# Kernel optimization log

Hardware: AMD Instinct MI355X
Metric: run time of the kernel (lower is better)

## Reference

```python
import jax, jax.numpy as jnp
import numpy as np

B, L = 8, 128
STATE_DIM, ACT_DIM = 6, 3
E = 256
D_MODEL = 256
N_LAYER = 4
D_INNER = 512   # expand=2
D_STATE = 16
DT_RANK = 16    # ceil(d_model/16)
D_CONV = 4
MAX_EP_LEN = 300
EPS = 1e-5


def rmsnorm(x, w):
    return x * jax.lax.rsqrt(jnp.mean(x * x, axis=-1, keepdims=True) + EPS) * w


def mamba_mixer(x, in_W, conv_w, conv_b, xproj_W, dt_W, dt_b, A_log, Dp, out_W):
    # x: (B, Lp, D_MODEL)
    bsz, Lp, _ = x.shape
    di = conv_w.shape[0]
    n = A_log.shape[-1]
    rk = dt_W.shape[0]
    xz = x @ in_W                              # (B, Lp, 2*di)
    xc, z = jnp.split(xz, 2, axis=-1)
    # depthwise causal conv1d, kernel D_CONV
    xc_t = xc.transpose(0, 2, 1)               # (B, di, Lp)
    xc_t = jax.lax.conv_general_dilated(
        xc_t, conv_w[:, None, :], (1,), [(D_CONV - 1, 0)],
        feature_group_count=di,
        dimension_numbers=('NCH', 'OIH', 'NCH')) + conv_b[None, :, None]
    xc = jax.nn.silu(xc_t.transpose(0, 2, 1))  # (B, Lp, di)
    proj = xc @ xproj_W                        # (B, Lp, rk + 2n)
    dt, Bm, Cm = jnp.split(proj, [rk, rk + n], axis=-1)
    dt = jax.nn.softplus(dt @ dt_W + dt_b)     # (B, Lp, di)
    A = -jnp.exp(A_log)                        # (di, n)

    def step(h, inp):
        dt_t, B_t, C_t, x_t = inp              # (B,di),(B,n),(B,n),(B,di)
        dA = jnp.exp(dt_t[:, :, None] * A)     # (B, di, n)
        h = dA * h + (dt_t * x_t)[:, :, None] * B_t[:, None, :]
        y = jnp.einsum('bdn,bn->bd', h, C_t)
        return h, y

    h0 = jnp.zeros((bsz, di, n), x.dtype)
    _, ys = jax.lax.scan(step, h0, (dt.transpose(1, 0, 2), Bm.transpose(1, 0, 2),
                                    Cm.transpose(1, 0, 2), xc.transpose(1, 0, 2)))
    y = ys.transpose(1, 0, 2) + xc * Dp        # (B, Lp, di)
    y = y * jax.nn.silu(z)
    return y @ out_W


def setup_inputs():
    key = jax.random.key(0)
    ks = jax.random.split(key, 24)
    s = 0.05
    inp = {}
    inp['states'] = jax.random.normal(ks[0], (B, L, STATE_DIM), jnp.float32)
    inp['actions'] = jax.random.normal(ks[1], (B, L, ACT_DIM), jnp.float32)
    inp['goal'] = jax.random.normal(ks[2], (B, L, STATE_DIM), jnp.float32)
    inp['timesteps'] = jax.random.randint(ks[3], (B, L), 0, MAX_EP_LEN)
    inp['te_W'] = jax.random.normal(ks[4], (MAX_EP_LEN, E)) * 0.02
    inp['se_W'] = jax.random.normal(ks[5], (STATE_DIM, E)) * s
    inp['se_b'] = jnp.zeros((E,))
    inp['ge_W'] = jax.random.normal(ks[6], (STATE_DIM, E)) * s
    inp['ge_b'] = jnp.zeros((E,))
    inp['ae_W'] = jax.random.normal(ks[7], (ACT_DIM, E)) * s
    inp['ae_b'] = jnp.zeros((E,))
    inp['bb_in_W'] = jax.random.normal(ks[8], (E, D_MODEL)) * s
    inp['bb_in_b'] = jnp.zeros((D_MODEL,))
    inp['norm_w'] = jnp.ones((N_LAYER, D_MODEL))
    inp['in_proj_W'] = jax.random.normal(ks[9], (N_LAYER, D_MODEL, 2 * D_INNER)) * s
    inp['conv_w'] = jax.random.normal(ks[10], (N_LAYER, D_INNER, D_CONV)) * s
    inp['conv_b'] = jnp.zeros((N_LAYER, D_INNER))
    inp['xproj_W'] = jax.random.normal(ks[11], (N_LAYER, D_INNER, DT_RANK + 2 * D_STATE)) * s
    inp['dt_W'] = jax.random.normal(ks[12], (N_LAYER, DT_RANK, D_INNER)) * s
    inp['dt_b'] = jnp.full((N_LAYER, D_INNER), float(np.log(np.expm1(0.01))), jnp.float32)
    inp['A_log'] = jnp.log(jnp.tile(jnp.arange(1, D_STATE + 1, dtype=jnp.float32), (N_LAYER, D_INNER, 1)))
    inp['Dp'] = jnp.ones((N_LAYER, D_INNER))
    inp['out_W'] = jax.random.normal(ks[13], (N_LAYER, D_INNER, D_MODEL)) * s / np.sqrt(N_LAYER)
    inp['fnorm_w'] = jnp.ones((D_MODEL,))
    inp['ps_W'] = jax.random.normal(ks[14], (D_MODEL, STATE_DIM)) * s
    inp['ps_b'] = jnp.zeros((STATE_DIM,))
    inp['pa_W'] = jax.random.normal(ks[15], (D_MODEL, ACT_DIM)) * s
    inp['pa_b'] = jnp.zeros((ACT_DIM,))
    return inp


def reference(states, actions, goal, timesteps, te_W, se_W, se_b, ge_W, ge_b,
              ae_W, ae_b, bb_in_W, bb_in_b, norm_w, in_proj_W, conv_w, conv_b,
              xproj_W, dt_W, dt_b, A_log, Dp, out_W, fnorm_w, ps_W, ps_b, pa_W, pa_b):
    bsz, Ls, _ = states.shape
    se = states @ se_W + se_b
    ge = goal @ ge_W + ge_b
    ae = actions @ ae_W + ae_b
    te = te_W[timesteps]                       # (B, L, E)
    se = se + te
    ae = ae + te
    ge = ge + te
    # interleave (g, s, a) per timestep -> (B, 3L, E)
    u = jnp.stack((ge, se, ae), axis=1).transpose(0, 2, 1, 3).reshape(bsz, 3 * Ls, E)
    residual = u @ bb_in_W + bb_in_b
    for i in range(norm_w.shape[0]):
        xn = rmsnorm(residual, norm_w[i])
        residual = residual + mamba_mixer(xn, in_proj_W[i], conv_w[i], conv_b[i],
                                          xproj_W[i], dt_W[i], dt_b[i], A_log[i],
                                          Dp[i], out_W[i])
    y = rmsnorm(residual, fnorm_w)
    y = y.reshape(bsz, Ls, 3, y.shape[-1]).transpose(0, 2, 1, 3)  # (B, 3, L, D)
    state_preds = y[:, -1] @ ps_W + ps_b       # from action-slot tokens
    action_preds = jnp.tanh(y[:, -2] @ pa_W + pa_b)  # from state-slot tokens
    return (state_preds, action_preds)
```

## Files before the change

### kernel.cpp

```cpp
#include <hip/hip_runtime.h>
#include <hip/hip_bf16.h>
#include <math.h>

#define BB 8
#define LL 128
#define SS 384
#define BT 3072
#define EE 256
#define DM 256
#define DI 512
#define DSTATE 16
#define RK 16
#define NL 4

typedef unsigned short u16;
typedef __attribute__((ext_vector_type(8))) short short8;
typedef __attribute__((ext_vector_type(4))) float f32x4;

__device__ __forceinline__ float bf(const u16 v){
    union { unsigned u; float f; } c; c.u = ((unsigned)v) << 16; return c.f;
}
__device__ __forceinline__ u16 f2bf(float f){
    union { float f; unsigned u; } c; c.f = f;
    unsigned x = c.u;
    unsigned r = (x >> 16) & 1u;
    x += 0x7fffu + r;
    return (u16)(x >> 16);
}
__device__ __forceinline__ unsigned pack2(float a, float b){
    return ((unsigned)f2bf(a)) | (((unsigned)f2bf(b)) << 16);
}
__device__ __forceinline__ int get_flag(const unsigned* nwraw){
    return (nwraw[0] == 0x3F800000u) ? 0 : 1;
}

#define SWZ_NB 848
#define CNV_NB 64

__device__ __constant__ int g_soff[13] = {0, 0, 262144, 524288, 786432,
                                          0, 131072, 262144, 393216,
                                          0, 24576, 49152, 73728};

struct SwzDesc { const void* src; u16* dst; int K; int N; int frags; };
struct PrepArgs {
    const void* csrc[23]; int cn[23]; int coff[23];
    SwzDesc sd[13];
};

__global__ __launch_bounds__(256) void k_prep(PrepArgs a,
                                              const unsigned* __restrict__ nwraw,
                                              float* __restrict__ dst){
    const int f = get_flag(nwraw);
    const int bk = blockIdx.x;
    if (bk < SWZ_NB){
        int gid = bk*256 + threadIdx.x;
        #pragma unroll 1
        for (int s = 0; s < 13; ++s){
            int fr = a.sd[s].frags;
            if (gid < fr){
                const int N = a.sd[s].N;
                const int l = gid & 63;
                const int rest = gid >> 6;
                const int kcn = a.sd[s].K >> 5;
                const int kc = rest % kcn;
                const int nt = rest / kcn;
                const int n  = nt*16 + (l & 15);
                const int k0 = kc*32 + (l >> 4)*8;
                u16 tmp[8];
                if (f){
                    const u16* src = (const u16*)a.sd[s].src;
                    #pragma unroll
                    for (int j = 0; j < 8; ++j) tmp[j] = src[(size_t)(k0+j)*N + n];
                } else {
                    const float* src = (const float*)((const char*)a.sd[s].src
                                                      + (size_t)g_soff[s]*2);
                    #pragma unroll
                    for (int j = 0; j < 8; ++j) tmp[j] = f2bf(src[(size_t)(k0+j)*N + n]);
                }
                *(short8*)(a.sd[s].dst + (size_t)gid*8) = *(short8*)tmp;
                return;
            }
            gid -= fr;
        }
    } else {
        const int stride = CNV_NB * 256;
        const int tid0 = (bk - SWZ_NB)*256 + threadIdx.x;
        #pragma unroll 1
        for (int s = 0; s < 23; ++s){
            const int n = a.cn[s];
            float* d = dst + a.coff[s];
            if (f){
                const u16* p = (const u16*)a.csrc[s];
                for (int i = tid0; i < n; i += stride) d[i] = bf(p[i]);
            } else {
                const float* p = (const float*)a.csrc[s];
                for (int i = tid0; i < n; i += stride) d[i] = p[i];
            }
        }
    }
}

__global__ __launch_bounds__(256) void k_embed_mfma(
    const float* __restrict__ states, const float* __restrict__ actions,
    const float* __restrict__ goal, const int* __restrict__ tsteps,
    const float* __restrict__ te_W, const float* __restrict__ se_W, const float* __restrict__ se_b,
    const float* __restrict__ ge_W, const float* __restrict__ ge_b,
    const float* __restrict__ ae_W, const float* __restrict__ ae_b,
    const u16* __restrict__ bbsw, const float* __restrict__ bb_b,
    float* __restrict__ residual)
{
    __shared__ u16 sA[32*264];
    const int tid = threadIdx.x;
    {
        const int m = tid >> 3, p = tid & 7, e0 = p*32;
        const int token = blockIdx.x*32 + m;
        const int b = token / SS, t = token % SS;
        const int slot = t % 3, step = t / 3;
        const int ts = tsteps[b*LL + step];
        float v[32];
        const float* tp = te_W + ts*EE + e0;
        #pragma unroll
        for (int i = 0; i < 8; ++i) *(float4*)(&v[i*4]) = *(const float4*)(tp + i*4);
        const float *bias, *Wp, *g; int nk;
        if (slot == 0){ bias = ge_b; Wp = ge_W; g = goal    + (b*LL+step)*6; nk = 6; }
        else if (slot == 1){ bias = se_b; Wp = se_W; g = states + (b*LL+step)*6; nk = 6; }
        else { bias = ae_b; Wp = ae_W; g = actions + (b*LL+step)*3; nk = 3; }
        #pragma unroll
        for (int i = 0; i < 8; ++i){
            float4 bv = *(const float4*)(bias + e0 + i*4);
            v[i*4]+=bv.x; v[i*4+1]+=bv.y; v[i*4+2]+=bv.z; v[i*4+3]+=bv.w;
        }
        for (int k = 0; k < nk; ++k){
            float gv = g[k];
            const float* wr = Wp + k*EE + e0;
            #pragma unroll
            for (int i = 0; i < 8; ++i){
                float4 wv = *(const float4*)(wr + i*4);
                v[i*4]+=gv*wv.x; v[i*4+1]+=gv*wv.y; v[i*4+2]+=gv*wv.z; v[i*4+3]+=gv*wv.w;
            }
        }
        unsigned* dp = (unsigned*)sA + (m*264 + e0)/2;
        #pragma unroll
        for (int i = 0; i < 16; ++i) dp[i] = pack2(v[2*i], v[2*i+1]);
    }
    __syncthreads();
    const int w = tid >> 6, l = tid & 63;
    const int mt = w >> 1, nq = w & 1;
    f32x4 acc[4] = {{0,0,0,0},{0,0,0,0},{0,0,0,0},{0,0,0,0}};
    const u16* ap0 = sA + (mt*16 + (l&15))*264 + (l>>4)*8;
    #pragma unroll
    for (int kc = 0; kc < 8; ++kc){
        short8 a = *(const short8*)(ap0 + kc*32);
        #pragma unroll
        for (int nt = 0; nt < 4; ++nt){
            int ntg = blockIdx.y*8 + nq*4 + nt;
            short8 b8 = *(const short8*)(bbsw + ((size_t)(ntg*8 + kc)*64 + l)*8);
            acc[nt] = __builtin_amdgcn_mfma_f32_16x16x32_bf16(a, b8, acc[nt], 0,0,0);
        }
    }
    const int mrow0 = blockIdx.x*32 + mt*16 + (l>>4)*4;
    #pragma unroll
    for (int nt = 0; nt < 4; ++nt){
        int col = (blockIdx.y*8 + nq*4 + nt)*16 + (l&15);
        float bb = bb_b[col];
        #pragma unroll
        for (int r = 0; r < 4; ++r)
            residual[(mrow0+r)*DM + col] = acc[nt][r] + bb;
    }
}

__global__ __launch_bounds__(256) void k_rms_inproj_mfma(
    const float* __restrict__ residual, const float* __restrict__ norm_w,
    const u16* __restrict__ Wsw,
    float* __restrict__ xc_raw, float* __restrict__ sz)
{
    __shared__ u16 sA[32*264];
    const int tid = threadIdx.x;
    {
        const int m = tid >> 3, p = tid & 7, e0 = p*32;
        const int row = blockIdx.x*32 + m;
        float v[32];
        const float* rp = residual + row*DM + e0;
        #pragma unroll
        for (int i = 0; i < 8; ++i) *(float4*)(&v[i*4]) = *(const float4*)(rp + i*4);
        float s = 0.f;
        #pragma unroll
        for (int i = 0; i < 32; ++i) s += v[i]*v[i];
        s += __shfl_xor(s,1,64); s += __shfl_xor(s,2,64); s += __shfl_xor(s,4,64);
        const float scale = rsqrtf(s*(1.f/DM) + 1e-5f);
        const float* nwp = norm_w + e0;
        unsigned* dp = (unsigned*)sA + (m*264 + e0)/2;
        #pragma unroll
        for (int i = 0; i < 16; ++i)
            dp[i] = pack2(v[2*i]*scale*nwp[2*i], v[2*i+1]*scale*nwp[2*i+1]);
    }
    __syncthreads();
    const int w = tid >> 6, l = tid & 63;
    const int mt = w >> 1, nq = w & 1;
    f32x4 acc[4] = {{0,0,0,0},{0,0,0,0},{0,0,0,0},{0,0,0,0}};
    const u16* ap0 = sA + (mt*16 + (l&15))*264 + (l>>4)*8;
    #pragma unroll
    for (int kc = 0; kc < 8; ++kc){
        short8 a = *(const short8*)(ap0 + kc*32);
        #pragma unroll
        for (int nt = 0; nt < 4; ++nt){
            int ntg = blockIdx.y*8 + nq*4 + nt;
            short8 b8 = *(const short8*)(Wsw + ((size_t)(ntg*8 + kc)*64 + l)*8);
            acc[nt] = __builtin_amdgcn_mfma_f32_16x16x32_bf16(a, b8, acc[nt], 0,0,0);
        }
    }
    const int mrow0 = blockIdx.x*32 + mt*16 + (l>>4)*4;
    if (blockIdx.y < 4){
        #pragma unroll
        for (int nt = 0; nt < 4; ++nt){
            int col = (blockIdx.y*8 + nq*4 + nt)*16 + (l&15);
            #pragma unroll
            for (int r = 0; r < 4; ++r)
                xc_raw[(mrow0+r)*DI + col] = acc[nt][r];
        }
    } else {
        #pragma unroll
        for (int nt = 0; nt < 4; ++nt){
            int col = (blockIdx.y*8 + nq*4 + nt)*16 + (l&15) - DI;
            #pragma unroll
            for (int r = 0; r < 4; ++r){
                float z = acc[nt][r];
                sz[(mrow0+r)*DI + col] = z / (1.f + __expf(-z));
            }
        }
    }
}

__global__ __launch_bounds__(256) void k_conv_mfma(
    const float* __restrict__ xc_raw,
    const float* __restrict__ conv_w, const float* __restrict__ conv_b,
    const u16* __restrict__ xpsw,
    const float* __restrict__ dt_W, const float* __restrict__ dt_b,
    float* __restrict__ xc, float* __restrict__ dtBC, float* __restrict__ dt)
{
    __shared__ u16 sxc[16*520];
    __shared__ float sdtbc[16*64];
    const int tid = threadIdx.x;
    const int base = blockIdx.x * 16;
    const int t0 = base % SS;

    #pragma unroll
    for (int half = 0; half < 2; ++half){
        const int d = tid + half*256;
        const float w0 = conv_w[d*4+0], w1 = conv_w[d*4+1];
        const float w2 = conv_w[d*4+2], w3 = conv_w[d*4+3];
        const float cb = conv_b[d];
        const float* rp = xc_raw + (size_t)base*DI + d;
        float xm3=0.f, xm2=0.f, xm1=0.f;
        if (t0 > 0){
            xm3 = rp[-3*DI]; xm2 = rp[-2*DI]; xm1 = rp[-DI];
        }
        #pragma unroll
        for (int tk = 0; tk < 16; ++tk){
            float x0 = rp[tk*DI];
            float a = cb + w0*xm3 + w1*xm2 + w2*xm1 + w3*x0;
            float s = a / (1.f + __expf(-a));
            xc[(size_t)(base+tk)*DI + d] = s;
            sxc[tk*520 + d] = f2bf(s);
            xm3 = xm2; xm2 = xm1; xm1 = x0;
        }
    }
    __syncthreads();

    const int w = tid >> 6, l = tid & 63;
    if (w < 3){
        f32x4 acc = {0,0,0,0};
        const u16* ap0 = sxc + (l&15)*520 + (l>>4)*8;
        #pragma unroll
        for (int kc = 0; kc < 16; ++kc){
            short8 a = *(const short8*)(ap0 + kc*32);
            short8 b8 = *(const short8*)(xpsw + ((size_t)(w*16 + kc)*64 + l)*8);
            acc = __builtin_amdgcn_mfma_f32_16x16x32_bf16(a, b8, acc, 0,0,0);
        }
        #pragma unroll
        for (int r = 0; r < 4; ++r)
            sdtbc[((l>>4)*4 + r)*64 + w*16 + (l&15)] = acc[r];
    }
    __syncthreads();

    #pragma unroll
    for (int r = 0; r < 2; ++r){
        int i = tid + r*256;
        int t = i >> 5, j = i & 31;
        dtBC[(size_t)(base+t)*48 + 16 + j] = sdtbc[t*64 + 16 + j];
    }

    #pragma unroll
    for (int half = 0; half < 2; ++half){
        const int d = tid + half*256;
        const float db = dt_b[d];
        float wr[16];
        #pragma unroll
        for (int r = 0; r < 16; ++r) wr[r] = dt_W[r*DI + d];
        #pragma unroll
        for (int tk = 0; tk < 16; ++tk){
            float a = db;
            #pragma unroll
            for (int r = 0; r < 16; ++r) a += sdtbc[tk*64 + r] * wr[r];
            float sp = (a > 15.f) ? a : __logf(1.f + __expf(a));
            dt[(size_t)(base+tk)*DI + d] = sp;
        }
    }
}

#define CT 32
#define NCH (SS/CT)

__global__ __launch_bounds__(256) void k_scan(
    const float* __restrict__ dt, const float* __restrict__ dtBC,
    const float* __restrict__ xc,
    const float* __restrict__ A_log, const float* __restrict__ Dp,
    float* __restrict__ y)
{
    __shared__ float s_dtx[2][CT*32];
    __shared__ float s_xc [2][CT*16];
    __shared__ float s_B [2][CT*16];
    __shared__ float s_C [2][CT*16];
    __shared__ float s_p [CT*16*17];
    __shared__ float s_Dp[16];

    const int tid = threadIdx.x;
    const int bk  = blockIdx.x;
    const int b   = bk >> 5;
    const int dg  = bk & 31;
    const int dgb = dg*16;
    const int ld  = tid >> 4, n = tid & 15;
    const int d   = dgb + ld;

    const float A = -__expf(A_log[d*DSTATE + n]);
    const size_t tokbase = (size_t)b*SS;

    float r_dt[2], r_xc[2], r_bc[4];

    auto issue_loads = [&](int c){
        const int t0 = c*CT;
        #pragma unroll
        for (int r = 0; r < 2; ++r){
            int e = tid + r*256;
            int t = e >> 4, dd = e & 15;
            size_t g = (tokbase + t0 + t)*DI + dgb + dd;
            r_dt[r] = dt[g];
            r_xc[r] = xc[g];
        }
        #pragma unroll
        for (int r = 0; r < 4; ++r){
            int e = tid + r*256;
            int t = e >> 5, j = e & 31;
            r_bc[r] = dtBC[(tokbase + t0 + t)*48 + 16 + j];
        }
    };
    auto commit = [&](int bu){
        #pragma unroll
        for (int r = 0; r < 2; ++r){
            int e = tid + r*256;
            int t = e >> 4, dd = e & 15;
            s_dtx[bu][t*32 + dd*2]     = r_dt[r];
            s_dtx[bu][t*32 + dd*2 + 1] = r_dt[r]*r_xc[r];
            s_xc[bu][e] = r_xc[r];
        }
        #pragma unroll
        for (int r = 0; r < 4; ++r){
            int e = tid + r*256;
            int t = e >> 5, j = e & 31;
            if (j < 16) s_B[bu][t*16 + j]      = r_bc[r];
            else        s_C[bu][t*16 + (j-16)] = r_bc[r];
        }
    };

    issue_loads(0);
    commit(0);
    if (tid < 16) s_Dp[tid] = Dp[dgb + tid];

    float h = 0.f;
    int buf = 0;
    for (int c = 0; c < NCH; ++c){
        __syncthreads();
        if (c+1 < NCH) issue_loads(c+1);
        const float* pdx = s_dtx[buf] + ld*2;
        const float* pB  = s_B[buf];
        const float* pC  = s_C[buf];
        float* pp = s_p + ld*17 + n;
        #pragma unroll
        for (int t = 0; t < CT; ++t){
            float2 dx = *(const float2*)(pdx + t*32);
            float Bv  = pB[t*16 + n];
            float dA  = __expf(dx.x * A);
            h = dA*h + dx.y*Bv;
            pp[t*272] = h * pC[t*16 + n];
        }
        __syncthreads();
        {
            const int t0 = c*CT;
            const float* pxc = s_xc[buf];
            #pragma unroll
            for (int r = 0; r < 2; ++r){
                int e = tid + r*256;
                int t = e >> 4, dd = e & 15;
                const float* q = s_p + e*17;
                float s = 0.f;
                #pragma unroll
                for (int k = 0; k < 16; ++k) s += q[k];
                y[(tokbase + t0 + t)*DI + dgb + dd] = s + pxc[e]*s_Dp[dd];
            }
        }
        if (c+1 < NCH) commit(buf^1);
        buf ^= 1;
    }
}

__global__ __launch_bounds__(256) void k_out_rms(
    const float* __restrict__ y, const float* __restrict__ szb,
    const u16* __restrict__ Wout, float* __restrict__ residual,
    const float* __restrict__ norm_w, const u16* __restrict__ Win,
    float* __restrict__ xc_raw, float* __restrict__ sz,
    int do_rms)
{
    __shared__ u16 sA[16*520];
    __shared__ float sRes[16*264];
    const int tid = threadIdx.x;
    const int base = blockIdx.x*16;
    {
        const int m = tid >> 4, p = tid & 15, e0 = p*32;
        const float* yp = y   + (size_t)(base+m)*DI + e0;
        const float* sp = szb + (size_t)(base+m)*DI + e0;
        unsigned* dp = (unsigned*)sA + (m*520 + e0)/2;
        #pragma unroll
        for (int i = 0; i < 8; ++i){
            float4 yv = *(const float4*)(yp + i*4);
            float4 sv = *(const float4*)(sp + i*4);
            dp[i*2]   = pack2(yv.x*sv.x, yv.y*sv.y);
            dp[i*2+1] = pack2(yv.z*sv.z, yv.w*sv.w);
        }
    }
    __syncthreads();
    const int w = tid >> 6, l = tid & 63;
    {
        f32x4 acc[4] = {{0,0,0,0},{0,0,0,0},{0,0,0,0},{0,0,0,0}};
        const u16* ap0 = sA + (l&15)*520 + (l>>4)*8;
        #pragma unroll
        for (int kc = 0; kc < 16; ++kc){
            short8 a = *(const short8*)(ap0 + kc*32);
            #pragma unroll
            for (int i = 0; i < 4; ++i){
                int ntg = w*4 + i;
                short8 b8 = *(const short8*)(Wout + ((size_t)(ntg*16 + kc)*64 + l)*8);
                acc[i] = __builtin_amdgcn_mfma_f32_16x16x32_bf16(a, b8, acc[i], 0,0,0);
            }
        }
        const int mrow0 = (l>>4)*4;
        #pragma unroll
        for (int i = 0; i < 4; ++i){
            int col = (w*4+i)*16 + (l&15);
            #pragma unroll
            for (int r = 0; r < 4; ++r){
                float v = residual[(base+mrow0+r)*DM + col] + acc[i][r];
                residual[(base+mrow0+r)*DM + col] = v;
                if (do_rms) sRes[(mrow0+r)*264 + col] = v;
            }
        }
    }
    if (!do_rms) return;
    __syncthreads();
    {
        const int m = tid >> 4, p = tid & 15;
        const float* rr = sRes + m*264 + p*16;
        float v[16];
        float ss = 0.f;
        #pragma unroll
        for (int i = 0; i < 16; ++i){ v[i] = rr[i]; ss += v[i]*v[i]; }
        ss += __shfl_xor(ss,1,64); ss += __shfl_xor(ss,2,64);
        ss += __shfl_xor(ss,4,64); ss += __shfl_xor(ss,8,64);
        const float scale = rsqrtf(ss*(1.f/DM) + 1e-5f);
        const float* nw = norm_w + p*16;
        unsigned* dp = (unsigned*)sA + (m*264 + p*16)/2;
        #pragma unroll
        for (int i = 0; i < 8; ++i)
            dp[i] = pack2(v[2*i]*scale*nw[2*i], v[2*i+1]*scale*nw[2*i+1]);
    }
    __syncthreads();
    {
        f32x4 acc[16];
        #pragma unroll
        for (int i = 0; i < 16; ++i) acc[i] = {0,0,0,0};
        const u16* ap0 = sA + (l&15)*264 + (l>>4)*8;
        #pragma unroll
        for (int kc = 0; kc < 8; ++kc){
            short8 a = *(const short8*)(ap0 + kc*32);
            #pragma unroll
            for (int i = 0; i < 16; ++i){
                int ntg = w*16 + i;
                short8 b8 = *(const short8*)(Win + ((size_t)(ntg*8 + kc)*64 + l)*8);
                acc[i] = __builtin_amdgcn_mfma_f32_16x16x32_bf16(a, b8, acc[i], 0,0,0);
            }
        }
        const int mrow0 = (l>>4)*4;
        #pragma unroll
        for (int i = 0; i < 16; ++i){
            int col = (w*16+i)*16 + (l&15);
            if (col < DI){
                #pragma unroll
                for (int r = 0; r < 4; ++r)
                    xc_raw[(size_t)(base+mrow0+r)*DI + col] = acc[i][r];
            } else {
                #pragma unroll
                for (int r = 0; r < 4; ++r){
                    float z = acc[i][r];
                    sz[(size_t)(base+mrow0+r)*DI + col - DI] = z / (1.f + __expf(-z));
                }
            }
        }
    }
}

__global__ __launch_bounds__(256) void k_heads(
    const float* __restrict__ residual, const float* __restrict__ fnorm_w,
    const float* __restrict__ ps_W, const float* __restrict__ ps_b,
    const float* __restrict__ pa_W, const float* __restrict__ pa_b,
    const unsigned* __restrict__ nwraw, void* __restrict__ out)
{
    __shared__ float x1[DM], x2[DM];
    __shared__ float sc[2];
    __shared__ float part[2][4];
    const int tid = threadIdx.x;
    const int bl = blockIdx.x;
    const int b = bl >> 7, l = bl & 127;
    const int fl = get_flag(nwraw);
    const int tok1 = b*SS + 3*l + 1;
    const int tok2 = tok1 + 1;
    float v1 = residual[tok1*DM + tid];
    float v2 = residual[tok2*DM + tid];
    {
        float s1 = v1*v1, s2 = v2*v2;
        #pragma unroll
        for (int off = 32; off >= 1; off >>= 1){
            s1 += __shfl_xor(s1, off, 64);
            s2 += __shfl_xor(s2, off, 64);
        }
        if ((tid & 63) == 0){ part[0][tid>>6] = s1; part[1][tid>>6] = s2; }
    }
    __syncthreads();
    if (tid < 2){
        float s = part[tid][0]+part[tid][1]+part[tid][2]+part[tid][3];
        sc[tid] = rsqrtf(s * (1.f/DM) + 1e-5f);
    }
    __syncthreads();
    float nw = fnorm_w[tid];
    x1[tid] = v1 * sc[0] * nw;
    x2[tid] = v2 * sc[1] * nw;
    __syncthreads();
    const int wv = tid >> 6, ln = tid & 63;
    for (int oi = wv; oi < 9; oi += 4){
        float a = 0.f;
        if (oi < 6){
            #pragma unroll
            for (int k = 0; k < 4; ++k){ int e = ln + 64*k; a += x2[e] * ps_W[e*6 + oi]; }
        } else {
            int j = oi - 6;
            #pragma unroll
            for (int k = 0; k < 4; ++k){ int e = ln + 64*k; a += x1[e] * pa_W[e*3 + j]; }
        }
        #pragma unroll
        for (int off = 32; off >= 1; off >>= 1) a += __shfl_xor(a, off, 64);
        if (ln == 0){
            float r; int idx;
            if (oi < 6){
                r = a + ps_b[oi];
                idx = (b*LL + l)*6 + oi;
            } else {
                int j = oi - 6;
                r = tanhf(a + pa_b[j]);
                idx = BB*LL*6 + (b*LL + l)*3 + j;
            }
            if (fl) ((u16*)out)[idx] = f2bf(r);
            else    ((float*)out)[idx] = r;
        }
    }
}

extern "C" void kernel_launch(void* const* d_in, const int* in_sizes, int n_in,
                              void* d_out, int out_size, void* d_ws, size_t ws_size,
                              hipStream_t stream)
{
    const int* tsteps = (const int*)d_in[3];
    const unsigned* nwraw = (const unsigned*)d_in[13];

    float* fin = (float*)d_ws;

    const int cidx[23] = {0,1,2,4,5,6,7,8,9,10,12,13,15,16,18,19,20,21,23,24,25,26,27};
    PrepArgs pa;
    const float* fp[28];
    for (int i = 0; i < 28; ++i) fp[i] = nullptr;
    int cur = 0;
    for (int i = 0; i < 23; ++i){
        int gi = cidx[i];
        pa.csrc[i] = d_in[gi];
        pa.cn[i]   = in_sizes[gi];
        pa.coff[i] = cur;
        fp[gi] = fin + cur;
        cur += in_sizes[gi];
        cur = (cur + 3) & ~3;
    }
    float* act = fin + cur;

    float* residual = act;            act += BT*DM;
    float* xc_raw   = act;            act += BT*DI;
    float* sz       = act;            act += BT*DI;
    float* xc       = act;            act += BT*DI;
    float* dtbuf    = act;            act += BT*DI;
    float* ybuf     = act;            act += BT*DI;
    float* dtBC     = act;            act += BT*48;

    u16* wsb    = (u16*)act;
    u16* bb_sw  = wsb;
    u16* in_sw  = bb_sw + 65536;
    u16* out_sw = in_sw + 4*262144;
    u16* xp_sw  = out_sw + 4*131072;

    const int soff[13] = {0, 0, 262144, 524288, 786432,
                          0, 131072, 262144, 393216,
                          0, 24576, 49152, 73728};
    pa.sd[0] = { d_in[11], bb_sw, 256, 256, (256/16)*(256/32)*64 };
    for (int i = 0; i < 4; ++i)
        pa.sd[1+i] = { d_in[14], in_sw + i*262144, 256, 1024,
                       (1024/16)*(256/32)*64 };
    for (int i = 0; i < 4; ++i)
        pa.sd[5+i] = { d_in[22], out_sw + i*131072, 512, 256,
                       (256/16)*(512/32)*64 };
    for (int i = 0; i < 4; ++i)
        pa.sd[9+i] = { d_in[17], xp_sw + i*24576, 512, 48,
                       (48/16)*(512/32)*64 };
    for (int i = 0; i < 13; ++i)
        pa.sd[i].src = (const void*)((const char*)pa.sd[i].src + (size_t)soff[i]*2);

    k_prep<<<SWZ_NB + CNV_NB, 256, 0, stream>>>(pa, nwraw, fin);

    k_embed_mfma<<<dim3(96,2), 256, 0, stream>>>(fp[0], fp[1], fp[2], tsteps,
        fp[4], fp[5], fp[6], fp[7], fp[8], fp[9], fp[10], bb_sw, fp[12], residual);

    k_rms_inproj_mfma<<<dim3(96,8), 256, 0, stream>>>(residual, fp[13],
        in_sw, xc_raw, sz);

    for (int lyr = 0; lyr < NL; ++lyr){
        k_conv_mfma<<<BT/16, 256, 0, stream>>>(xc_raw, fp[15] + lyr*DI*4,
            fp[16] + lyr*DI, xp_sw + lyr*24576, fp[18] + lyr*RK*DI, fp[19] + lyr*DI,
            xc, dtBC, dtbuf);
        k_scan<<<256, 256, 0, stream>>>(dtbuf, dtBC, xc,
            fp[20] + lyr*DI*DSTATE, fp[21] + lyr*DI, ybuf);
        if (lyr < NL-1){
            k_out_rms<<<192, 256, 0, stream>>>(ybuf, sz, out_sw + lyr*131072,
                residual, fp[13] + (lyr+1)*DM, in_sw + (lyr+1)*262144,
                xc_raw, sz, 1);
        } else {
            k_out_rms<<<192, 256, 0, stream>>>(ybuf, sz, out_sw + lyr*131072,
                residual, fp[13], in_sw, xc_raw, sz, 0);
        }
    }
    k_heads<<<BB*LL, 256, 0, stream>>>(residual, fp[23], fp[24], fp[25], fp[26], fp[27],
                                       nwraw, (u16*)d_out);
}
```

Baseline: 448.8 us.

## Split fused out-proj/RMSNorm/in-proj kernel into separate wider-grid kernels

Replaces the fused out-projection + RMSNorm + next-layer in-projection kernel (192 blocks) with a standalone out-projection kernel on a 192x2 grid. The existing 96x8-grid rmsnorm+in-projection kernel is now launched at the start of every layer. This spreads the GEMM work over many more blocks to fill the GPU's compute units better. The cost is extra kernel launches and a round trip of the residual through global memory between the two stages.

```diff
diff --git a/kernel.cpp b/kernel.cpp
--- a/kernel.cpp
+++ b/kernel.cpp
@@ -413,21 +413,17 @@
     }
 }
 
-__global__ __launch_bounds__(256) void k_out_rms(
+__global__ __launch_bounds__(256) void k_outproj_mfma(
     const float* __restrict__ y, const float* __restrict__ szb,
-    const u16* __restrict__ Wout, float* __restrict__ residual,
-    const float* __restrict__ norm_w, const u16* __restrict__ Win,
-    float* __restrict__ xc_raw, float* __restrict__ sz,
-    int do_rms)
+    const u16* __restrict__ Wsw, float* __restrict__ residual)
 {
     __shared__ u16 sA[16*520];
-    __shared__ float sRes[16*264];
     const int tid = threadIdx.x;
-    const int base = blockIdx.x*16;
     {
         const int m = tid >> 4, p = tid & 15, e0 = p*32;
-        const float* yp = y   + (size_t)(base+m)*DI + e0;
-        const float* sp = szb + (size_t)(base+m)*DI + e0;
+        const int row = blockIdx.x*16 + m;
+        const float* yp = y   + (size_t)row*DI + e0;
+        const float* sp = szb + (size_t)row*DI + e0;
         unsigned* dp = (unsigned*)sA + (m*520 + e0)/2;
         #pragma unroll
         for (int i = 0; i < 8; ++i){
@@ -439,81 +435,25 @@
     }
     __syncthreads();
     const int w = tid >> 6, l = tid & 63;
-    {
-        f32x4 acc[4] = {{0,0,0,0},{0,0,0,0},{0,0,0,0},{0,0,0,0}};
-        const u16* ap0 = sA + (l&15)*520 + (l>>4)*8;
-        #pragma unroll
-        for (int kc = 0; kc < 16; ++kc){
-            short8 a = *(const short8*)(ap0 + kc*32);
-            #pragma unroll
-            for (int i = 0; i < 4; ++i){
-                int ntg = w*4 + i;
-                short8 b8 = *(const short8*)(Wout + ((size_t)(ntg*16 + kc)*64 + l)*8);
-                acc[i] = __builtin_amdgcn_mfma_f32_16x16x32_bf16(a, b8, acc[i], 0,0,0);
-            }
-        }
-        const int mrow0 = (l>>4)*4;
-        #pragma unroll
-        for (int i = 0; i < 4; ++i){
-            int col = (w*4+i)*16 + (l&15);
-            #pragma unroll
-            for (int r = 0; r < 4; ++r){
-                float v = residual[(base+mrow0+r)*DM + col] + acc[i][r];
-                residual[(base+mrow0+r)*DM + col] = v;
-                if (do_rms) sRes[(mrow0+r)*264 + col] = v;
-            }
-        }
-    }
-    if (!do_rms) return;
-    __syncthreads();
-    {
-        const int m = tid >> 4, p = tid & 15;
-        const float* rr = sRes + m*264 + p*16;
-        float v[16];
-        float ss = 0.f;
-        #pragma unroll
-        for (int i = 0; i < 16; ++i){ v[i] = rr[i]; ss += v[i]*v[i]; }
-        ss += __shfl_xor(ss,1,64); ss += __shfl_xor(ss,2,64);
-        ss += __shfl_xor(ss,4,64); ss += __shfl_xor(ss,8,64);
-        const float scale = rsqrtf(ss*(1.f/DM) + 1e-5f);
-        const float* nw = norm_w + p*16;
-        unsigned* dp = (unsigned*)sA + (m*264 + p*16)/2;
-        #pragma unroll
-        for (int i = 0; i < 8; ++i)
-            dp[i] = pack2(v[2*i]*scale*nw[2*i], v[2*i+1]*scale*nw[2*i+1]);
-    }
-    __syncthreads();
-    {
-        f32x4 acc[16];
-        #pragma unroll
-        for (int i = 0; i < 16; ++i) acc[i] = {0,0,0,0};
-        const u16* ap0 = sA + (l&15)*264 + (l>>4)*8;
-        #pragma unroll
-        for (int kc = 0; kc < 8; ++kc){
-            short8 a = *(const short8*)(ap0 + kc*32);
-            #pragma unroll
-            for (int i = 0; i < 16; ++i){
-                int ntg = w*16 + i;
-                short8 b8 = *(const short8*)(Win + ((size_t)(ntg*8 + kc)*64 + l)*8);
-                acc[i] = __builtin_amdgcn_mfma_f32_16x16x32_bf16(a, b8, acc[i], 0,0,0);
-            }
-        }
-        const int mrow0 = (l>>4)*4;
-        #pragma unroll
-        for (int i = 0; i < 16; ++i){
-            int col = (w*16+i)*16 + (l&15);
-            if (col < DI){
-                #pragma unroll
-                for (int r = 0; r < 4; ++r)
-                    xc_raw[(size_t)(base+mrow0+r)*DI + col] = acc[i][r];
-            } else {
-                #pragma unroll
-                for (int r = 0; r < 4; ++r){
-                    float z = acc[i][r];
-                    sz[(size_t)(base+mrow0+r)*DI + col - DI] = z / (1.f + __expf(-z));
-                }
-            }
-        }
+    f32x4 acc[2] = {{0,0,0,0},{0,0,0,0}};
+    const u16* ap0 = sA + (l&15)*520 + (l>>4)*8;
+    #pragma unroll
+    for (int kc = 0; kc < 16; ++kc){
+        short8 a = *(const short8*)(ap0 + kc*32);
+        #pragma unroll
+        for (int i = 0; i < 2; ++i){
+            int ntg = blockIdx.y*8 + w*2 + i;
+            short8 b8 = *(const short8*)(Wsw + ((size_t)(ntg*16 + kc)*64 + l)*8);
+            acc[i] = __builtin_amdgcn_mfma_f32_16x16x32_bf16(a, b8, acc[i], 0,0,0);
+        }
+    }
+    const int mrow0 = blockIdx.x*16 + (l>>4)*4;
+    #pragma unroll
+    for (int i = 0; i < 2; ++i){
+        int col = (blockIdx.y*8 + w*2 + i)*16 + (l&15);
+        #pragma unroll
+        for (int r = 0; r < 4; ++r)
+            residual[(mrow0+r)*DM + col] += acc[i][r];
     }
 }
 
@@ -642,23 +582,16 @@
     k_embed_mfma<<<dim3(96,2), 256, 0, stream>>>(fp[0], fp[1], fp[2], tsteps,
         fp[4], fp[5], fp[6], fp[7], fp[8], fp[9], fp[10], bb_sw, fp[12], residual);
 
-    k_rms_inproj_mfma<<<dim3(96,8), 256, 0, stream>>>(residual, fp[13],
-        in_sw, xc_raw, sz);
-
     for (int lyr = 0; lyr < NL; ++lyr){
+        k_rms_inproj_mfma<<<dim3(96,8), 256, 0, stream>>>(residual, fp[13] + lyr*DM,
+            in_sw + lyr*262144, xc_raw, sz);
         k_conv_mfma<<<BT/16, 256, 0, stream>>>(xc_raw, fp[15] + lyr*DI*4,
             fp[16] + lyr*DI, xp_sw + lyr*24576, fp[18] + lyr*RK*DI, fp[19] + lyr*DI,
             xc, dtBC, dtbuf);
         k_scan<<<256, 256, 0, stream>>>(dtbuf, dtBC, xc,
             fp[20] + lyr*DI*DSTATE, fp[21] + lyr*DI, ybuf);
-        if (lyr < NL-1){
-            k_out_rms<<<192, 256, 0, stream>>>(ybuf, sz, out_sw + lyr*131072,
-                residual, fp[13] + (lyr+1)*DM, in_sw + (lyr+1)*262144,
-                xc_raw, sz, 1);
-        } else {
-            k_out_rms<<<192, 256, 0, stream>>>(ybuf, sz, out_sw + lyr*131072,
-                residual, fp[13], in_sw, xc_raw, sz, 0);
-        }
+        k_outproj_mfma<<<dim3(192,2), 256, 0, stream>>>(ybuf, sz,
+            out_sw + lyr*131072, residual);
     }
     k_heads<<<BB*LL, 256, 0, stream>>>(residual, fp[23], fp[24], fp[25], fp[26], fp[27],
                                        nwraw, (u16*)d_out);
```

Measured after the change: 369.7 us. -17.6%, faster.
